# Kernel tuning notes

Hardware: AMD Instinct MI355X
Metric: run time of the kernel (lower is better)

Reference implementation:

```python
import jax, jax.numpy as jnp
import numpy as np

N, C, H, W = 8, 64, 128, 128
CO, K = 64, 3
BN_EPS = 1e-5
POW_EPS = 1e-12  # keeps |x|**alpha differentiable at 0


def setup_inputs() -> dict:
    key = jax.random.key(0)
    k1, k2, k3, k4 = jax.random.split(key, 4)
    x = jax.random.normal(k1, (N, C, H, W), jnp.float32)
    weight = jax.random.normal(k2, (CO, C, K, K), jnp.float32) * 0.1
    gamma = 1.0 + 0.1 * jax.random.normal(k3, (C,), jnp.float32)
    beta = 0.1 * jax.random.normal(k4, (C,), jnp.float32)
    alpha = jnp.float32(1.0)  # learnable power of PowerActivation (AdderSR)
    return {"x": x, "weight": weight, "gamma": gamma, "beta": beta, "alpha": alpha}


def adder2d(x, weight):
    """AdderNet conv: out[n,co,h,w] = -sum_{ci,kh,kw} |patch - W[co,ci,kh,kw]|."""
    co, ci, kh, kw = weight.shape
    # [N, C*kh*kw, H, W], channel-major feature layout matches weight.reshape(co, -1)
    patches = jax.lax.conv_general_dilated_patches(
        x, (kh, kw), (1, 1), padding=((1, 1), (1, 1)))
    wflat = weight.reshape(co, -1)

    def per_out_channel(w):  # w: [C*kh*kw]
        return -jnp.sum(jnp.abs(patches - w[None, :, None, None]), axis=1)  # [N,H,W]

    out = jax.lax.map(per_out_channel, wflat)  # [CO, N, H, W] (sequential -> bounded memory)
    return jnp.transpose(out, (1, 0, 2, 3))    # [N, CO, H, W]


def reference(x, weight, gamma, beta, alpha):
    y = adder2d(x, weight) + x  # residual add
    # BatchNorm2d in training mode: batch statistics over (N, H, W)
    mean = jnp.mean(y, axis=(0, 2, 3), keepdims=True)
    var = jnp.var(y, axis=(0, 2, 3), keepdims=True)
    y = (y - mean) * jax.lax.rsqrt(var + BN_EPS)
    y = y * gamma[None, :, None, None] + beta[None, :, None, None]
    # PowerActivation: sign(x) * |x|^alpha (learnable alpha)
    return jnp.sign(y) * jnp.power(jnp.abs(y) + POW_EPS, alpha)
```

## Files before the change

kernel.cpp:

```cpp
#include <hip/hip_runtime.h>
#include <math.h>

#define N_   8
#define C_   64
#define H_   128
#define W_   128
#define HW_  (H_ * W_)
#define CHW_ (C_ * HW_)
#define K_   3
#define CI_TILE 4
#define CO_BLK  8
#define N_CG    (C_ / CO_BLK)
#define TILE_H 16
#define TILE_W 32
#define HALO_H (TILE_H + 2)
#define HALO_W (TILE_W + 2)
#define XSTR   36
#define CISZ   (HALO_H * XSTR)
#define PLANE  (HALO_H * HALO_W)
#define NSLOT  5
#define WROW 12
#define WCI  (CO_BLK * WROW)
#define WSTRIDE (C_ * K_ * K_)
#define BN_EPS 1e-5
#define POW_EPS 1e-12f

#define MAC_TERM(accv, wv, xvk) do { float t_;                         \
    asm("v_sub_f32 %1, %2, %3\n\t"                                     \
        "v_add_f32 %0, %0, |%1|"                                       \
        : "+v"(accv), "=&v"(t_)                                        \
        : "v"(wv), "v"(xvk));                                          \
  } while (0)

__global__ __launch_bounds__(128, 4) void adder_kernel(
    const float* __restrict__ x, const float* __restrict__ weight,
    float* __restrict__ y, double* __restrict__ sums)
{
    __shared__ __align__(16) float sx[CI_TILE * CISZ];
    __shared__ __align__(16) float wl[CI_TILE * WCI];
    __shared__ float red[CO_BLK][2][2];

    const int tx = threadIdx.x & 15;
    const int ty = threadIdx.x >> 4;
    const int tile_h = blockIdx.x >> 2;
    const int tile_w = blockIdx.x & 3;
    const int n   = blockIdx.y;
    const int co0 = blockIdx.z * CO_BLK;
    const int h0 = tile_h * TILE_H;
    const int w0 = tile_w * TILE_W;

    float a00[CO_BLK], a01[CO_BLK], a10[CO_BLK], a11[CO_BLK];
#pragma unroll
    for (int j = 0; j < CO_BLK; ++j) { a00[j]=0.f; a01[j]=0.f; a10[j]=0.f; a11[j]=0.f; }

    const float* xn = x + n * CHW_;

    int lx[NSLOT], gx[NSLOT];
#pragma unroll
    for (int s = 0; s < NSLOT; ++s) {
        int idx = threadIdx.x + s * 128;
        if (idx < PLANE) {
            int r = idx / HALO_W, c = idx - r * HALO_W;
            int gh = h0 + r - 1, gw = w0 + c - 1;
            lx[s] = r * XSTR + c;
            gx[s] = ((unsigned)gh < (unsigned)H_ && (unsigned)gw < (unsigned)W_)
                    ? (gh * W_ + gw) : -1;
        } else { lx[s] = -1; gx[s] = -1; }
    }
    int wlo = -1, wgo = 0;
    if (threadIdx.x < CO_BLK * 9) {
        int co = threadIdx.x / 9, k = threadIdx.x - co * 9;
        wlo = co * WROW + k;
        wgo = (co0 + co) * WSTRIDE + k;
    }

    float rs[CI_TILE * NSLOT];
    float rw[CI_TILE];

#define ISSUE_STAGE(CBN) do {                                            \
        const float* xp_ = xn + (CBN) * HW_;                             \
        _Pragma("unroll")                                                \
        for (int ci_ = 0; ci_ < CI_TILE; ++ci_) {                        \
            _Pragma("unroll")                                            \
            for (int s_ = 0; s_ < NSLOT; ++s_)                           \
                rs[ci_ * NSLOT + s_] = (gx[s_] >= 0)                     \
                    ? xp_[ci_ * HW_ + gx[s_]] : 0.f;                     \
        }                                                                \
        if (wlo >= 0) {                                                  \
            _Pragma("unroll")                                            \
            for (int ci_ = 0; ci_ < CI_TILE; ++ci_)                      \
                rw[ci_] = weight[wgo + ((CBN) + ci_) * 9];               \
        }                                                                \
    } while (0)

    ISSUE_STAGE(0);

    for (int cb = 0; cb < C_; cb += CI_TILE) {
        __syncthreads();
#pragma unroll
        for (int ci = 0; ci < CI_TILE; ++ci) {
#pragma unroll
            for (int s = 0; s < NSLOT; ++s)
                if (lx[s] >= 0)
                    sx[ci * CISZ + lx[s]] = rs[ci * NSLOT + s];
        }
        if (wlo >= 0) {
#pragma unroll
            for (int ci = 0; ci < CI_TILE; ++ci)
                wl[ci * WCI + wlo] = rw[ci];
        }
        if (cb + CI_TILE < C_) ISSUE_STAGE(cb + CI_TILE);
        __syncthreads();

#pragma unroll 1
        for (int ci = 0; ci < CI_TILE; ++ci) {
            const float* sxc = &sx[ci * CISZ];
            float xv[4][4];
#pragma unroll
            for (int r = 0; r < 4; ++r) {
                float2 a = *(const float2*)(sxc + (2 * ty + r) * XSTR + 2 * tx);
                float2 b = *(const float2*)(sxc + (2 * ty + r) * XSTR + 2 * tx + 2);
                xv[r][0] = a.x; xv[r][1] = a.y; xv[r][2] = b.x; xv[r][3] = b.y;
            }

            const float* wrow = &wl[ci * WCI];
#pragma unroll
            for (int j = 0; j < CO_BLK; ++j) {
                float4 wa = *(const float4*)(wrow + j * WROW);
                float4 wb = *(const float4*)(wrow + j * WROW + 4);
                float  w8 = wrow[j * WROW + 8];
                MAC_TERM(a00[j], wa.x, xv[0][0]); MAC_TERM(a01[j], wa.x, xv[0][1]);
                MAC_TERM(a10[j], wa.x, xv[1][0]); MAC_TERM(a11[j], wa.x, xv[1][1]);
                MAC_TERM(a00[j], wa.y, xv[0][1]); MAC_TERM(a01[j], wa.y, xv[0][2]);
                MAC_TERM(a10[j], wa.y, xv[1][1]); MAC_TERM(a11[j], wa.y, xv[1][2]);
                MAC_TERM(a00[j], wa.z, xv[0][2]); MAC_TERM(a01[j], wa.z, xv[0][3]);
                MAC_TERM(a10[j], wa.z, xv[1][2]); MAC_TERM(a11[j], wa.z, xv[1][3]);
                MAC_TERM(a00[j], wa.w, xv[1][0]); MAC_TERM(a01[j], wa.w, xv[1][1]);
                MAC_TERM(a10[j], wa.w, xv[2][0]); MAC_TERM(a11[j], wa.w, xv[2][1]);
                MAC_TERM(a00[j], wb.x, xv[1][1]); MAC_TERM(a01[j], wb.x, xv[1][2]);
                MAC_TERM(a10[j], wb.x, xv[2][1]); MAC_TERM(a11[j], wb.x, xv[2][2]);
                MAC_TERM(a00[j], wb.y, xv[1][2]); MAC_TERM(a01[j], wb.y, xv[1][3]);
                MAC_TERM(a10[j], wb.y, xv[2][2]); MAC_TERM(a11[j], wb.y, xv[2][3]);
                MAC_TERM(a00[j], wb.z, xv[2][0]); MAC_TERM(a01[j], wb.z, xv[2][1]);
                MAC_TERM(a10[j], wb.z, xv[3][0]); MAC_TERM(a11[j], wb.z, xv[3][1]);
                MAC_TERM(a00[j], wb.w, xv[2][1]); MAC_TERM(a01[j], wb.w, xv[2][2]);
                MAC_TERM(a10[j], wb.w, xv[3][1]); MAC_TERM(a11[j], wb.w, xv[3][2]);
                MAC_TERM(a00[j], w8,   xv[2][2]); MAC_TERM(a01[j], w8,   xv[2][3]);
                MAC_TERM(a10[j], w8,   xv[3][2]); MAC_TERM(a11[j], w8,   xv[3][3]);
            }
        }
    }

    const int r0 = h0 + 2 * ty, c0 = w0 + 2 * tx;
    float* yo = y + n * CHW_ + co0 * HW_ + r0 * W_ + c0;
    const float* xrp = xn + co0 * HW_ + r0 * W_ + c0;
    const int lane = threadIdx.x & 63;
    const int wid  = threadIdx.x >> 6;

#pragma unroll
    for (int j = 0; j < CO_BLK; ++j) {
        float2 rv0 = *(const float2*)(xrp + j * HW_);
        float2 rv1 = *(const float2*)(xrp + j * HW_ + W_);
        float v00 = -a00[j] + rv0.x, v01 = -a01[j] + rv0.y;
        float v10 = -a10[j] + rv1.x, v11 = -a11[j] + rv1.y;
        float2 o0; o0.x = v00; o0.y = v01;
        float2 o1; o1.x = v10; o1.y = v11;
        *(float2*)(yo + j * HW_)      = o0;
        *(float2*)(yo + j * HW_ + W_) = o1;
        float s  = v00 + v01 + v10 + v11;
        float ss = v00 * v00 + v01 * v01 + v10 * v10 + v11 * v11;
#pragma unroll
        for (int off = 32; off > 0; off >>= 1) {
            s  += __shfl_down(s, off);
            ss += __shfl_down(ss, off);
        }
        if (lane == 0) { red[j][0][wid] = s; red[j][1][wid] = ss; }
    }
    __syncthreads();
    if (threadIdx.x < CO_BLK) {
        int j = threadIdx.x;
        float S  = red[j][0][0] + red[j][0][1];
        float SS = red[j][1][0] + red[j][1][1];
        atomicAdd(&sums[co0 + j], (double)S);
        atomicAdd(&sums[C_ + co0 + j], (double)SS);
    }
}

__global__ void finalize_kernel(const double* __restrict__ sums,
                                const float* __restrict__ gamma,
                                const float* __restrict__ beta,
                                float* __restrict__ sc)
{
    const int c = threadIdx.x;
    const double cnt = (double)(N_ * HW_);
    double mean = sums[c] / cnt;
    double var  = sums[C_ + c] / cnt - mean * mean;
    float inv   = (float)(1.0 / sqrt(var + (double)BN_EPS));
    float scale = gamma[c] * inv;
    float shift = beta[c] - (float)mean * scale;
    sc[c]      = scale;
    sc[C_ + c] = shift;
}

__global__ __launch_bounds__(256) void apply_kernel(
    float* __restrict__ y, const float* __restrict__ sc,
    const float* __restrict__ alpha_p)
{
    const int idx = blockIdx.x * 256 + threadIdx.x;
    const float alpha = alpha_p[0];
    const int e0 = idx * 4;
    const int c = (e0 / HW_) & (C_ - 1);
    const float scale = sc[c];
    const float shift = sc[C_ + c];

    float4 v = reinterpret_cast<float4*>(y)[idx];
    float* pv = reinterpret_cast<float*>(&v);
    if (alpha == 1.0f) {
#pragma unroll
        for (int i = 0; i < 4; ++i)
            pv[i] = pv[i] * scale + shift;
    } else {
#pragma unroll
        for (int i = 0; i < 4; ++i) {
            float t = pv[i] * scale + shift;
            float sgn = (t > 0.f) ? 1.f : ((t < 0.f) ? -1.f : 0.f);
            pv[i] = sgn * powf(fabsf(t) + POW_EPS, alpha);
        }
    }
    reinterpret_cast<float4*>(y)[idx] = v;
}

extern "C" void kernel_launch(void* const* d_in, const int* in_sizes, int n_in,
                              void* d_out, int out_size, void* d_ws, size_t ws_size,
                              hipStream_t stream)
{
    const float* x      = (const float*)d_in[0];
    const float* weight = (const float*)d_in[1];
    const float* gamma  = (const float*)d_in[2];
    const float* beta   = (const float*)d_in[3];
    const float* alpha  = (const float*)d_in[4];
    float* out = (float*)d_out;

    double* sums = (double*)d_ws;
    float*  sc   = (float*)((char*)d_ws + 128 * sizeof(double));

    hipMemsetAsync(d_ws, 0, 128 * sizeof(double), stream);

    adder_kernel<<<dim3(32, N_, N_CG), 128, 0, stream>>>(x, weight, out, sums);
    finalize_kernel<<<1, C_, 0, stream>>>(sums, gamma, beta, sc);

    const int n4 = (N_ * CHW_) / 4;
    apply_kernel<<<n4 / 256, 256, 0, stream>>>(out, sc, alpha);
}
```

Measured before the change: 293.2 us.

## Double-buffer LDS input tiles with two channels per stage

Replaces the single LDS buffer of four input channels with two ping-pong buffers of two channels each. The next stage is written into the alternate buffer after compute, so each iteration needs one barrier instead of two. Weight loading is redistributed so all 128 threads load at most two weights each. The cost is twice as many loop iterations, more barriers in total, and a different LDS footprint and register count.

```diff
diff --git a/kernel.cpp b/kernel.cpp
--- a/kernel.cpp
+++ b/kernel.cpp
@@ -8,7 +8,7 @@
 #define HW_  (H_ * W_)
 #define CHW_ (C_ * HW_)
 #define K_   3
-#define CI_TILE 4
+#define CI2  2
 #define CO_BLK  8
 #define N_CG    (C_ / CO_BLK)
 #define TILE_H 16
@@ -36,8 +36,8 @@
     const float* __restrict__ x, const float* __restrict__ weight,
     float* __restrict__ y, double* __restrict__ sums)
 {
-    __shared__ __align__(16) float sx[CI_TILE * CISZ];
-    __shared__ __align__(16) float wl[CI_TILE * WCI];
+    __shared__ __align__(16) float sx[2][CI2 * CISZ];
+    __shared__ __align__(16) float wl[2][CI2 * WCI];
     __shared__ float red[CO_BLK][2][2];
 
     const int tx = threadIdx.x & 15;
@@ -67,54 +67,60 @@
                     ? (gh * W_ + gw) : -1;
         } else { lx[s] = -1; gx[s] = -1; }
     }
-    int wlo = -1, wgo = 0;
-    if (threadIdx.x < CO_BLK * 9) {
-        int co = threadIdx.x / 9, k = threadIdx.x - co * 9;
-        wlo = co * WROW + k;
-        wgo = (co0 + co) * WSTRIDE + k;
-    }
-
-    float rs[CI_TILE * NSLOT];
-    float rw[CI_TILE];
+    int wlo0, wgo0, wlo1 = -1, wgo1 = 0;
+    {
+        int i0 = threadIdx.x;
+        int ci = i0 / (CO_BLK * 9), r = i0 - ci * (CO_BLK * 9);
+        int co = r / 9, k = r - co * 9;
+        wlo0 = (ci * CO_BLK + co) * WROW + k;
+        wgo0 = (co0 + co) * WSTRIDE + ci * 9 + k;
+        int i1 = threadIdx.x + 128;
+        if (i1 < CI2 * CO_BLK * 9) {
+            ci = i1 / (CO_BLK * 9); r = i1 - ci * (CO_BLK * 9);
+            co = r / 9; k = r - co * 9;
+            wlo1 = (ci * CO_BLK + co) * WROW + k;
+            wgo1 = (co0 + co) * WSTRIDE + ci * 9 + k;
+        }
+    }
+
+    float rs[CI2 * NSLOT];
+    float rwA, rwB;
 
 #define ISSUE_STAGE(CBN) do {                                            \
         const float* xp_ = xn + (CBN) * HW_;                             \
         _Pragma("unroll")                                                \
-        for (int ci_ = 0; ci_ < CI_TILE; ++ci_) {                        \
+        for (int ci_ = 0; ci_ < CI2; ++ci_)                              \
             _Pragma("unroll")                                            \
             for (int s_ = 0; s_ < NSLOT; ++s_)                           \
                 rs[ci_ * NSLOT + s_] = (gx[s_] >= 0)                     \
                     ? xp_[ci_ * HW_ + gx[s_]] : 0.f;                     \
-        }                                                                \
-        if (wlo >= 0) {                                                  \
+        rwA = weight[wgo0 + (CBN) * 9];                                  \
+        if (wlo1 >= 0) rwB = weight[wgo1 + (CBN) * 9];                   \
+    } while (0)
+
+#define WRITE_STAGE(BUF) do {                                            \
+        _Pragma("unroll")                                                \
+        for (int ci_ = 0; ci_ < CI2; ++ci_)                              \
             _Pragma("unroll")                                            \
-            for (int ci_ = 0; ci_ < CI_TILE; ++ci_)                      \
-                rw[ci_] = weight[wgo + ((CBN) + ci_) * 9];               \
-        }                                                                \
+            for (int s_ = 0; s_ < NSLOT; ++s_)                           \
+                if (lx[s_] >= 0)                                         \
+                    sx[BUF][ci_ * CISZ + lx[s_]] = rs[ci_ * NSLOT + s_]; \
+        wl[BUF][wlo0] = rwA;                                             \
+        if (wlo1 >= 0) wl[BUF][wlo1] = rwB;                              \
     } while (0)
 
     ISSUE_STAGE(0);
-
-    for (int cb = 0; cb < C_; cb += CI_TILE) {
-        __syncthreads();
-#pragma unroll
-        for (int ci = 0; ci < CI_TILE; ++ci) {
-#pragma unroll
-            for (int s = 0; s < NSLOT; ++s)
-                if (lx[s] >= 0)
-                    sx[ci * CISZ + lx[s]] = rs[ci * NSLOT + s];
-        }
-        if (wlo >= 0) {
-#pragma unroll
-            for (int ci = 0; ci < CI_TILE; ++ci)
-                wl[ci * WCI + wlo] = rw[ci];
-        }
-        if (cb + CI_TILE < C_) ISSUE_STAGE(cb + CI_TILE);
-        __syncthreads();
+    WRITE_STAGE(0);
+    __syncthreads();
+
+    int cur = 0;
+    for (int cb = 0; cb < C_; cb += CI2) {
+        const bool more = (cb + CI2 < C_);
+        if (more) ISSUE_STAGE(cb + CI2);
 
 #pragma unroll 1
-        for (int ci = 0; ci < CI_TILE; ++ci) {
-            const float* sxc = &sx[ci * CISZ];
+        for (int ci = 0; ci < CI2; ++ci) {
+            const float* sxc = &sx[cur][ci * CISZ];
             float xv[4][4];
 #pragma unroll
             for (int r = 0; r < 4; ++r) {
@@ -123,7 +129,7 @@
                 xv[r][0] = a.x; xv[r][1] = a.y; xv[r][2] = b.x; xv[r][3] = b.y;
             }
 
-            const float* wrow = &wl[ci * WCI];
+            const float* wrow = &wl[cur][ci * WCI];
 #pragma unroll
             for (int j = 0; j < CO_BLK; ++j) {
                 float4 wa = *(const float4*)(wrow + j * WROW);
@@ -149,6 +155,12 @@
                 MAC_TERM(a10[j], w8,   xv[3][2]); MAC_TERM(a11[j], w8,   xv[3][3]);
             }
         }
+
+        if (more) {
+            WRITE_STAGE(cur ^ 1);
+            __syncthreads();
+            cur ^= 1;
+        }
     }
 
     const int r0 = h0 + 2 * ty, c0 = w0 + 2 * tx;
```

Measured after the change: 290.3 us. No clear change (-1.0%).
